# Optimization experiments

Hardware: AMD Instinct MI355X
Metric: run time of the kernel (lower is better)

Reference implementation:

```python
import jax, jax.numpy as jnp
import numpy as np

# Standard SMPL kinematic tree parents (kintree_table)
PARENTS = np.array([-1, 0, 0, 0, 1, 2, 3, 4, 5, 6, 7, 8, 9, 9, 9,
                    12, 13, 14, 16, 17, 18, 19, 20, 21])
NV, NJ, NB, NP = 6890, 24, 10, 207


def rodrigues(r):
    """Axis-angle [N,3] -> rotation matrices [N,3,3] (Rodrigues formula)."""
    theta = jnp.linalg.norm(r, axis=1, keepdims=True) + 1e-8  # [N,1]
    rh = r / theta                                            # [N,3]
    cos = jnp.cos(theta)[..., None]                           # [N,1,1]
    sin = jnp.sin(theta)[..., None]
    z = jnp.zeros_like(rh[:, 0])
    m = jnp.stack([z, -rh[:, 2], rh[:, 1],
                   rh[:, 2], z, -rh[:, 0],
                   -rh[:, 1], rh[:, 0], z], axis=1).reshape(-1, 3, 3)
    dot = rh[:, :, None] * rh[:, None, :]                     # outer product
    eye = jnp.eye(3, dtype=r.dtype)
    return cos * eye + (1.0 - cos) * dot + sin * m


def setup_inputs() -> dict:
    key = jax.random.key(0)
    ks = jax.random.split(key, 9)
    B = 512
    betas = jax.random.normal(ks[0], (B, NB), dtype=jnp.float32)
    thetas = jax.random.normal(ks[1], (B, NJ * 3), dtype=jnp.float32) * 0.3
    trans = jax.random.normal(ks[2], (B, 3), dtype=jnp.float32)
    scale = jnp.ones((1,), dtype=jnp.float32)
    v_template = jax.random.normal(ks[3], (NV, 3), dtype=jnp.float32)
    shapedirs = jax.random.normal(ks[4], (NV, 3, NB), dtype=jnp.float32) * 0.01
    posedirs = jax.random.normal(ks[5], (NV, 3, NP), dtype=jnp.float32) * 0.01
    Jr = jax.random.uniform(ks[6], (NJ, NV), dtype=jnp.float32)
    J_regressor = Jr / jnp.sum(Jr, axis=1, keepdims=True)
    w = jax.random.uniform(ks[7], (NV, NJ), dtype=jnp.float32)
    weights = w / jnp.sum(w, axis=1, keepdims=True)
    return {"betas": betas, "thetas": thetas, "trans": trans, "scale": scale,
            "v_template": v_template, "shapedirs": shapedirs,
            "posedirs": posedirs, "J_regressor": J_regressor,
            "weights": weights}


def reference(betas, thetas, trans, scale, v_template, shapedirs, posedirs,
              J_regressor, weights):
    B = betas.shape[0]
    dt = betas.dtype
    # Shape blend shapes: v_shaped [B, 6890, 3]
    v_shaped = jnp.einsum('bs,vcs->bvc', betas, shapedirs) + v_template
    # Rest-pose joints J(beta): [B, 24, 3]
    J = jnp.einsum('jv,bvc->bjc', J_regressor, v_shaped)
    # Local rotations from axis-angle, root scaled by `scale`
    lRs = rodrigues(thetas.reshape(-1, 3)).reshape(B, NJ, 3, 3)
    lRs = lRs.at[:, 0].multiply(scale[0])
    # Local joint offsets: root keeps J[:,0], children use J[i] - J[parent[i]]
    parents = jnp.asarray(PARENTS)
    t = J - J[:, jnp.clip(parents, 0)]
    t = t.at[:, 0].set(J[:, 0])
    # Local 4x4 transforms [B, 24, 4, 4]
    top = jnp.concatenate([lRs, t[..., None]], axis=3)          # [B,24,3,4]
    bottom = jnp.broadcast_to(jnp.array([0., 0., 0., 1.], dtype=dt),
                              (B, NJ, 1, 4))
    A = jnp.concatenate([top, bottom], axis=2)
    # Kinematic chain accumulation (fixed 24-joint tree)
    results = [A[:, 0]]
    for i in range(1, NJ):
        results.append(results[PARENTS[i]] @ A[:, i])
    stacked = jnp.stack(results, axis=1)                         # [B,24,4,4]
    # Remove rest-pose joint locations from translation column
    Jh = jnp.concatenate([J, jnp.zeros((B, NJ, 1), dtype=dt)], axis=2)
    deformed = jnp.einsum('bjxy,bjy->bjx', stacked, Jh)          # [B,24,4]
    G = stacked.at[..., 3].add(-deformed)
    # Pose blend shapes from non-root rotations
    lrotmin = (lRs[:, 1:] - jnp.eye(3, dtype=dt)).reshape(B, -1)  # [B,207]
    v_posed = v_shaped + jnp.einsum('bp,vcp->bvc', lrotmin, posedirs)
    # Linear blend skinning
    T = jnp.einsum('bjxy,vj->bvxy', G, weights)                  # [B,6890,4,4]
    vh = jnp.concatenate([v_posed, jnp.ones((B, NV, 1), dtype=dt)], axis=2)
    v = jnp.einsum('bvxy,bvy->bvx', T, vh)[:, :, :3]
    result = v + trans[:, None, :]
    joints = jnp.einsum('jv,bvc->bjc', J_regressor, result)
    return result, joints
```

## Files before the change

kernel.cpp:

```cpp
#include <hip/hip_runtime.h>

#define NVERT 6890
#define NJNT  24
#define NBETA 10
#define NPOSE 207
#define NBATCH 512
#define KPAD 224
#define MROWS 20736
#define NVC (NVERT * 3)

typedef __attribute__((ext_vector_type(8))) short short8;
typedef __attribute__((ext_vector_type(4))) float floatx4;

__constant__ int c_par[NJNT]   = {-1,0,0,0,1,2,3,4,5,6,7,8,9,9,9,12,13,14,16,17,18,19,20,21};
__constant__ int c_depth[NJNT] = { 0,1,1,1,2,2,2,3,3,3,4,4,4,4,4,5,5,5,6,6,7,7,8,8};

static __device__ __forceinline__ unsigned short f2bf(float x) {
  union { float f; unsigned u; } v; v.f = x;
  unsigned r = (v.u + 0x7FFFu + ((v.u >> 16) & 1u)) >> 16;
  return (unsigned short)r;
}
static __device__ __forceinline__ float bf2f(unsigned short h) {
  union { unsigned u; float f; } v; v.u = (unsigned)h << 16;
  return v.f;
}

__global__ __launch_bounds__(256) void k_buildA(
    const float* __restrict__ pdir, const float* __restrict__ sd,
    const float* __restrict__ vt, unsigned short* __restrict__ AT) {
  const int idx = blockIdx.x * 256 + threadIdx.x;
  const int kk = idx & 31;
  const int row = (idx >> 5) % MROWS;
  const int kt = idx / (MROWS * 32);
  const int k = kt * 32 + kk;
  float val = 0.f;
  if (row < NVC) {
    if (k < NPOSE)            val = pdir[(size_t)row * NPOSE + k];
    else if (k < NPOSE + 10)  val = sd[(size_t)row * 10 + (k - NPOSE)];
    else if (k == NPOSE + 10) val = vt[row];
  }
  AT[idx] = f2bf(val);
}

__global__ __launch_bounds__(256) void k_buildW(
    const float* __restrict__ wgt, unsigned short* __restrict__ W16) {
  const int idx = blockIdx.x * 256 + threadIdx.x;
  const int v = idx >> 6, c = idx & 63, j = c & 31, h = c >> 5;
  const float w = (v < NVERT && j < 24) ? wgt[(size_t)v * 24 + j] : 0.f;
  const unsigned short hi = f2bf(w);
  W16[idx] = h ? f2bf(w - bf2f(hi)) : hi;
}

__global__ __launch_bounds__(256) void k_jreg1(
    const float* __restrict__ Jr, const float* __restrict__ vt,
    const float* __restrict__ sd, float* __restrict__ wsJP) {
  const int jc = blockIdx.x, j = jc / 3, c = jc % 3;
  const int v0 = blockIdx.y * 864;
  const int vend = min(NVERT, v0 + 864);
  const int tid = threadIdx.x;
  float acc[11];
  #pragma unroll
  for (int k = 0; k < 11; ++k) acc[k] = 0.f;
  for (int v = v0 + tid; v < vend; v += 256) {
    const float w = Jr[j * NVERT + v];
    acc[0] += w * vt[v * 3 + c];
    const float* s = sd + (size_t)v * 30 + c * 10;
    #pragma unroll
    for (int k = 0; k < 10; ++k) acc[1 + k] += w * s[k];
  }
  #pragma unroll
  for (int off = 32; off > 0; off >>= 1) {
    #pragma unroll
    for (int k = 0; k < 11; ++k) acc[k] += __shfl_down(acc[k], off, 64);
  }
  __shared__ float red[4][11];
  const int lane = tid & 63, wv = tid >> 6;
  if (lane == 0) {
    #pragma unroll
    for (int k = 0; k < 11; ++k) red[wv][k] = acc[k];
  }
  __syncthreads();
  if (tid == 0) {
    #pragma unroll
    for (int k = 0; k < 11; ++k)
      wsJP[(size_t)(blockIdx.y * 72 + jc) * 11 + k] =
          red[0][k] + red[1][k] + red[2][k] + red[3][k];
  }
}

__global__ __launch_bounds__(256, 2) void k_chain3(
    const float* __restrict__ betas, const float* __restrict__ thetas,
    const float* __restrict__ scale, const float* __restrict__ trans,
    const float* __restrict__ wsJP,
    unsigned short* __restrict__ BT, unsigned short* __restrict__ G16) {
  __shared__ __align__(16) float sJ[792];
  __shared__ __align__(16) float sJJ[4][72];
  __shared__ __align__(16) float sM[4][288];
  __shared__ __align__(16) unsigned short sG[4][1024];
  __shared__ __align__(16) unsigned short sB[4][KPAD];

  const int tid = threadIdx.x;
  const int wv = tid >> 6, lane = tid & 63;
  const int b = blockIdx.x * 4 + wv;

  if (tid < 72) {
    #pragma unroll
    for (int k = 0; k < 11; ++k) {
      float s = 0.f;
      #pragma unroll
      for (int c8 = 0; c8 < 8; ++c8) s += wsJP[(size_t)(c8 * 72 + tid) * 11 + k];
      if (k == 0) sJ[tid] = s;
      else        sJ[72 + tid * 10 + (k - 1)] = s;
    }
  }
  #pragma unroll
  for (int r = 0; r < 4; ++r) {
    sG[wv][lane * 16 + r * 4 + 0] = 0; sG[wv][lane * 16 + r * 4 + 1] = 0;
    sG[wv][lane * 16 + r * 4 + 2] = 0; sG[wv][lane * 16 + r * 4 + 3] = 0;
  }
  __syncthreads();

  float R[9], t[3], M[12], Jx = 0.f, Jy = 0.f, Jz = 0.f;
  const int i = lane;
  if (i < NJNT) {
    #pragma unroll
    for (int c = 0; c < 3; ++c) {
      float a = sJ[i * 3 + c];
      const float* d = sJ + 72 + (i * 3 + c) * 10;
      #pragma unroll
      for (int s = 0; s < NBETA; ++s) a += d[s] * betas[b * NBETA + s];
      if (c == 0) Jx = a; else if (c == 1) Jy = a; else Jz = a;
    }
    sJJ[wv][i * 3 + 0] = Jx; sJJ[wv][i * 3 + 1] = Jy; sJJ[wv][i * 3 + 2] = Jz;
    const float rx = thetas[b * 72 + i * 3 + 0];
    const float ry = thetas[b * 72 + i * 3 + 1];
    const float rz = thetas[b * 72 + i * 3 + 2];
    const float th = sqrtf(rx * rx + ry * ry + rz * rz) + 1e-8f;
    const float inv = 1.f / th;
    const float x = rx * inv, y = ry * inv, z = rz * inv;
    const float cs = cosf(th), sn = sinf(th), omc = 1.f - cs;
    R[0] = cs + omc * x * x;     R[1] = omc * x * y - sn * z; R[2] = omc * x * z + sn * y;
    R[3] = omc * x * y + sn * z; R[4] = cs + omc * y * y;     R[5] = omc * y * z - sn * x;
    R[6] = omc * x * z - sn * y; R[7] = omc * y * z + sn * x; R[8] = cs + omc * z * z;
    if (i == 0) {
      const float sc = scale[0];
      #pragma unroll
      for (int k = 0; k < 9; ++k) R[k] *= sc;
    } else {
      #pragma unroll
      for (int k = 0; k < 9; ++k)
        sB[wv][(i - 1) * 9 + k] = f2bf(R[k] - ((k == 0 || k == 4 || k == 8) ? 1.f : 0.f));
    }
  }
  if (i == 0) {
    #pragma unroll
    for (int s = 0; s < NBETA; ++s) sB[wv][NPOSE + s] = f2bf(betas[b * NBETA + s]);
    sB[wv][NPOSE + 10] = 0x3F80;
    #pragma unroll
    for (int k = NPOSE + 11; k < KPAD; ++k) sB[wv][k] = 0;
  }
  __syncthreads();

  if (i < NJNT) {
    if (i == 0) { t[0] = Jx; t[1] = Jy; t[2] = Jz; }
    else {
      const int p = c_par[i];
      t[0] = Jx - sJJ[wv][p * 3 + 0];
      t[1] = Jy - sJJ[wv][p * 3 + 1];
      t[2] = Jz - sJJ[wv][p * 3 + 2];
    }
    if (i == 0) {
      #pragma unroll
      for (int r = 0; r < 3; ++r) {
        M[r*4+0] = R[r*3+0]; M[r*4+1] = R[r*3+1]; M[r*4+2] = R[r*3+2]; M[r*4+3] = t[r];
      }
      #pragma unroll
      for (int k = 0; k < 12; ++k) sM[wv][k] = M[k];
    }
  }
  __syncthreads();

  for (int lvl = 1; lvl <= 8; ++lvl) {
    if (i < NJNT && c_depth[i] == lvl) {
      const float* Mp = sM[wv] + c_par[i] * 12;
      #pragma unroll
      for (int r = 0; r < 3; ++r) {
        const float p0 = Mp[r*4+0], p1 = Mp[r*4+1], p2 = Mp[r*4+2], p3 = Mp[r*4+3];
        M[r*4+0] = p0*R[0] + p1*R[3] + p2*R[6];
        M[r*4+1] = p0*R[1] + p1*R[4] + p2*R[7];
        M[r*4+2] = p0*R[2] + p1*R[5] + p2*R[8];
        M[r*4+3] = p0*t[0] + p1*t[1] + p2*t[2] + p3;
      }
      #pragma unroll
      for (int k = 0; k < 12; ++k) sM[wv][i * 12 + k] = M[k];
    }
    __syncthreads();
  }

  if (i < NJNT) {
    #pragma unroll
    for (int r = 0; r < 3; ++r) {
      M[r*4+3] = M[r*4+3] - (M[r*4+0]*Jx + M[r*4+1]*Jy + M[r*4+2]*Jz)
               + trans[b * 3 + r];
    }
    #pragma unroll
    for (int e = 0; e < 12; ++e) {
      const float g = M[e];
      const unsigned short hi = f2bf(g);
      sG[wv][e * 32 + i]       = hi;
      sG[wv][512 + e * 32 + i] = f2bf(g - bf2f(hi));
    }
  }
  __syncthreads();

  *(uint4*)(G16 + (size_t)b * 1024 + lane * 16)     = *(uint4*)&sG[wv][lane * 16];
  *(uint4*)(G16 + (size_t)b * 1024 + lane * 16 + 8) = *(uint4*)&sG[wv][lane * 16 + 8];
  if (lane < 28)
    *(uint4*)(BT + ((size_t)(lane >> 2) * NBATCH + b) * 32 + (lane & 3) * 8) =
        *(uint4*)&sB[wv][lane * 8];
}

__global__ __launch_bounds__(256, 3) void k_skin4(
    const unsigned short* __restrict__ AT, const unsigned short* __restrict__ BT,
    const unsigned short* __restrict__ W16, const unsigned short* __restrict__ G16,
    float* __restrict__ out) {
  __shared__ __align__(16) char smem[33536];
  unsigned short* sAs = (unsigned short*)smem;
  unsigned short* sBs = (unsigned short*)(smem + 15360);
  float* sV           = (float*)smem;
  unsigned short* sG2 = (unsigned short*)(smem + 13056);

  const int tid = threadIdx.x;
  const int wv = tid >> 6, lane = tid & 63;
  const int q = lane >> 4, n = lane & 15;

  const int fb = blockIdx.x;
  const int vb = (fb & 7) * 108 + (fb >> 3);
  const int b0 = (vb & 7) * 64;
  const int by = vb >> 3;
  const int vc0 = by * 192;

  floatx4 acc[3][4];
  #pragma unroll
  for (int mt = 0; mt < 3; ++mt)
    #pragma unroll
    for (int nt = 0; nt < 4; ++nt) acc[mt][nt] = (floatx4)(0.f);

  const int srow = tid >> 2, sj = tid & 3;

  for (int kt = 0; kt < 7; ++kt) {
    if (kt) __syncthreads();
    #pragma unroll
    for (int it = 0; it < 3; ++it)
      *(uint4*)(sAs + (it * 64 + srow) * 40 + sj * 8) =
          *(const uint4*)(AT + ((size_t)kt * MROWS + vc0 + it * 64 + srow) * 32 + sj * 8);
    *(uint4*)(sBs + srow * 40 + sj * 8) =
        *(const uint4*)(BT + ((size_t)kt * NBATCH + b0 + srow) * 32 + sj * 8);
    __syncthreads();
    short8 af[3], bfr[4];
    #pragma unroll
    for (int mt = 0; mt < 3; ++mt)
      af[mt] = *(const short8*)(sAs + (48 * wv + 16 * mt + n) * 40 + q * 8);
    #pragma unroll
    for (int nt = 0; nt < 4; ++nt)
      bfr[nt] = *(const short8*)(sBs + (16 * nt + n) * 40 + q * 8);
    #pragma unroll
    for (int mt = 0; mt < 3; ++mt)
      #pragma unroll
      for (int nt = 0; nt < 4; ++nt)
        acc[mt][nt] = __builtin_amdgcn_mfma_f32_16x16x32_bf16(
            af[mt], bfr[nt], acc[mt][nt], 0, 0, 0);
  }

  short8 wh[4], wl[4];
  #pragma unroll
  for (int vt = 0; vt < 4; ++vt) {
    const unsigned short* wr = W16 + (size_t)(by * 64 + vt * 16 + n) * 64;
    wh[vt] = *(const short8*)(wr + q * 8);
    wl[vt] = *(const short8*)(wr + 32 + q * 8);
  }

  for (int nt = 0; nt < 4; ++nt) {
    for (int s = 0; s < 2; ++s) {
      __syncthreads();
      if (s == 0) {
        #pragma unroll
        for (int mt = 0; mt < 3; ++mt)
          #pragma unroll
          for (int r = 0; r < 4; ++r)
            sV[(48 * wv + 16 * mt + 4 * q + r) * 17 + n] = acc[mt][nt][r];
      }
      const int bg0 = b0 + nt * 16 + s * 8;
      for (int i = tid; i < 1024; i += 256) {
        const int row = i >> 2, c4 = i & 3;
        const int t = row >> 5, rem = row & 31;
        *(uint4*)(sG2 + row * 40 + c4 * 8) =
            *(const uint4*)(G16 + (size_t)(bg0 + t) * 1024 + rem * 32 + c4 * 8);
      }
      __syncthreads();
      #pragma unroll
      for (int bb = 0; bb < 2; ++bb) {
        const int t = wv * 2 + bb;
        const int col = s * 8 + t;
        const int bg = b0 + nt * 16 + col;
        const short8 gh = *(const short8*)(sG2 + (t * 32 + n) * 40 + q * 8);
        const short8 gl = *(const short8*)(sG2 + (t * 32 + 16 + n) * 40 + q * 8);
        #pragma unroll
        for (int vt = 0; vt < 4; ++vt) {
          floatx4 a2 = (floatx4)(0.f);
          a2 = __builtin_amdgcn_mfma_f32_16x16x32_bf16(gh, wl[vt], a2, 0, 0, 0);
          a2 = __builtin_amdgcn_mfma_f32_16x16x32_bf16(gl, wh[vt], a2, 0, 0, 0);
          a2 = __builtin_amdgcn_mfma_f32_16x16x32_bf16(gh, wh[vt], a2, 0, 0, 0);
          const float X = sV[(48 * vt + 3 * n + 0) * 17 + col];
          const float Y = sV[(48 * vt + 3 * n + 1) * 17 + col];
          const float Z = sV[(48 * vt + 3 * n + 2) * 17 + col];
          const float o = a2[0] * X + a2[1] * Y + a2[2] * Z + a2[3];
          const int vc = vc0 + 48 * vt + 3 * n + q;
          if (q < 3 && vc < NVC)
            out[(size_t)bg * NVC + vc] = o;
        }
      }
    }
  }
}

__global__ __launch_bounds__(256) void k_jnt1(
    const float* __restrict__ Jr, const float* __restrict__ res,
    float* __restrict__ wsJ2) {
  const int b0 = blockIdx.x * 2;
  const int chunk = blockIdx.y;
  const int v0 = chunk * 864;
  const int vend = min(NVERT, v0 + 864);
  const int lane = threadIdx.x & 63, wv = threadIdx.x >> 6;
  float acc[36];
  #pragma unroll
  for (int k = 0; k < 36; ++k) acc[k] = 0.f;
  const float* rA = res + (size_t)b0 * NVC;
  const float* rB = res + (size_t)(b0 + 1) * NVC;
  for (int v = v0 + lane; v < vend; v += 64) {
    const float a0 = rA[v * 3 + 0], a1 = rA[v * 3 + 1], a2 = rA[v * 3 + 2];
    const float e0 = rB[v * 3 + 0], e1 = rB[v * 3 + 1], e2 = rB[v * 3 + 2];
    #pragma unroll
    for (int k = 0; k < 6; ++k) {
      const int j = wv + 4 * k;
      const float w = Jr[j * NVERT + v];
      acc[k*6+0] += w * a0; acc[k*6+1] += w * a1; acc[k*6+2] += w * a2;
      acc[k*6+3] += w * e0; acc[k*6+4] += w * e1; acc[k*6+5] += w * e2;
    }
  }
  #pragma unroll
  for (int off = 32; off > 0; off >>= 1) {
    #pragma unroll
    for (int k = 0; k < 36; ++k) acc[k] += __shfl_down(acc[k], off, 64);
  }
  if (lane == 0) {
    #pragma unroll
    for (int k = 0; k < 6; ++k) {
      const int j = wv + 4 * k;
      float* d0 = wsJ2 + ((size_t)b0 * 8 + chunk) * 72 + j * 3;
      d0[0] = acc[k*6+0]; d0[1] = acc[k*6+1]; d0[2] = acc[k*6+2];
      float* d1 = wsJ2 + ((size_t)(b0 + 1) * 8 + chunk) * 72 + j * 3;
      d1[0] = acc[k*6+3]; d1[1] = acc[k*6+4]; d1[2] = acc[k*6+5];
    }
  }
}

__global__ __launch_bounds__(256) void k_jnt2(
    const float* __restrict__ wsJ2, float* __restrict__ joints) {
  const int idx = blockIdx.x * 256 + threadIdx.x;
  const int b = idx / 72, jc = idx - b * 72;
  float s = 0.f;
  #pragma unroll
  for (int c8 = 0; c8 < 8; ++c8)
    s += wsJ2[((size_t)b * 8 + c8) * 72 + jc];
  joints[idx] = s;
}

extern "C" void kernel_launch(void* const* d_in, const int* in_sizes, int n_in,
                              void* d_out, int out_size, void* d_ws, size_t ws_size,
                              hipStream_t stream) {
  const float* betas  = (const float*)d_in[0];
  const float* thetas = (const float*)d_in[1];
  const float* trans  = (const float*)d_in[2];
  const float* scale  = (const float*)d_in[3];
  const float* vtpl   = (const float*)d_in[4];
  const float* sd     = (const float*)d_in[5];
  const float* pdir   = (const float*)d_in[6];
  const float* Jr     = (const float*)d_in[7];
  const float* wgt    = (const float*)d_in[8];
  float* out = (float*)d_out;

  float* ws   = (float*)d_ws;
  float* wsJP = ws;
  unsigned short* AT  = (unsigned short*)(ws + 6336);
  unsigned short* BT  = AT + (size_t)MROWS * KPAD;
  unsigned short* W16 = BT + (size_t)NBATCH * KPAD;
  unsigned short* G16 = W16 + (size_t)6912 * 64;
  float* wsJ2 = (float*)AT;

  k_buildA<<<(MROWS * KPAD) / 256, 256, 0, stream>>>(pdir, sd, vtpl, AT);
  k_buildW<<<(6912 * 64) / 256, 256, 0, stream>>>(wgt, W16);
  k_jreg1<<<dim3(72, 8), 256, 0, stream>>>(Jr, vtpl, sd, wsJP);
  k_chain3<<<NBATCH / 4, 256, 0, stream>>>(betas, thetas, scale, trans, wsJP, BT, G16);
  k_skin4<<<864, 256, 0, stream>>>(AT, BT, W16, G16, out);
  k_jnt1<<<dim3(NBATCH / 2, 8), 256, 0, stream>>>(Jr, out, wsJ2);
  k_jnt2<<<(NBATCH * 72) / 256, 256, 0, stream>>>(wsJ2, out + (size_t)NBATCH * NVC);
}
```

Before: 171.5 us.

## Merge prep kernels into one launch and register-prefetch skin kernel tiles

The three preparation kernels (bf16 conversion of the blend-shape matrix, split-bf16 skinning weights, joint-regressor partial sums) become one launch whose block ranges select the task. This removes two launches and lets the independent tasks run concurrently. In the skinning kernel, the A/B K-tiles and the G transform tiles are now prefetched into registers one step ahead, so global loads overlap the MFMA work. The cost is higher register pressure, which may lower occupancy.

```diff
diff --git a/kernel.cpp b/kernel.cpp
--- a/kernel.cpp
+++ b/kernel.cpp
@@ -9,6 +9,10 @@
 #define MROWS 20736
 #define NVC (NVERT * 3)
 
+#define NBA 18144
+#define NBW 1728
+#define NJR 576
+
 typedef __attribute__((ext_vector_type(8))) short short8;
 typedef __attribute__((ext_vector_type(4))) float floatx4;
 
@@ -25,66 +29,67 @@
   return v.f;
 }
 
-__global__ __launch_bounds__(256) void k_buildA(
+__global__ __launch_bounds__(256) void k_prep(
     const float* __restrict__ pdir, const float* __restrict__ sd,
-    const float* __restrict__ vt, unsigned short* __restrict__ AT) {
-  const int idx = blockIdx.x * 256 + threadIdx.x;
-  const int kk = idx & 31;
-  const int row = (idx >> 5) % MROWS;
-  const int kt = idx / (MROWS * 32);
-  const int k = kt * 32 + kk;
-  float val = 0.f;
-  if (row < NVC) {
-    if (k < NPOSE)            val = pdir[(size_t)row * NPOSE + k];
-    else if (k < NPOSE + 10)  val = sd[(size_t)row * 10 + (k - NPOSE)];
-    else if (k == NPOSE + 10) val = vt[row];
-  }
-  AT[idx] = f2bf(val);
-}
-
-__global__ __launch_bounds__(256) void k_buildW(
-    const float* __restrict__ wgt, unsigned short* __restrict__ W16) {
-  const int idx = blockIdx.x * 256 + threadIdx.x;
-  const int v = idx >> 6, c = idx & 63, j = c & 31, h = c >> 5;
-  const float w = (v < NVERT && j < 24) ? wgt[(size_t)v * 24 + j] : 0.f;
-  const unsigned short hi = f2bf(w);
-  W16[idx] = h ? f2bf(w - bf2f(hi)) : hi;
-}
-
-__global__ __launch_bounds__(256) void k_jreg1(
-    const float* __restrict__ Jr, const float* __restrict__ vt,
-    const float* __restrict__ sd, float* __restrict__ wsJP) {
-  const int jc = blockIdx.x, j = jc / 3, c = jc % 3;
-  const int v0 = blockIdx.y * 864;
-  const int vend = min(NVERT, v0 + 864);
+    const float* __restrict__ vt, const float* __restrict__ wgt,
+    const float* __restrict__ Jr,
+    unsigned short* __restrict__ AT, unsigned short* __restrict__ W16,
+    float* __restrict__ wsJP) {
+  const int bx = blockIdx.x;
   const int tid = threadIdx.x;
-  float acc[11];
-  #pragma unroll
-  for (int k = 0; k < 11; ++k) acc[k] = 0.f;
-  for (int v = v0 + tid; v < vend; v += 256) {
-    const float w = Jr[j * NVERT + v];
-    acc[0] += w * vt[v * 3 + c];
-    const float* s = sd + (size_t)v * 30 + c * 10;
-    #pragma unroll
-    for (int k = 0; k < 10; ++k) acc[1 + k] += w * s[k];
-  }
-  #pragma unroll
-  for (int off = 32; off > 0; off >>= 1) {
-    #pragma unroll
-    for (int k = 0; k < 11; ++k) acc[k] += __shfl_down(acc[k], off, 64);
-  }
-  __shared__ float red[4][11];
-  const int lane = tid & 63, wv = tid >> 6;
-  if (lane == 0) {
-    #pragma unroll
-    for (int k = 0; k < 11; ++k) red[wv][k] = acc[k];
-  }
-  __syncthreads();
-  if (tid == 0) {
-    #pragma unroll
-    for (int k = 0; k < 11; ++k)
-      wsJP[(size_t)(blockIdx.y * 72 + jc) * 11 + k] =
-          red[0][k] + red[1][k] + red[2][k] + red[3][k];
+  if (bx < NBA) {
+    const int idx = bx * 256 + tid;
+    const int kk = idx & 31;
+    const int row = (idx >> 5) % MROWS;
+    const int kt = idx / (MROWS * 32);
+    const int k = kt * 32 + kk;
+    float val = 0.f;
+    if (row < NVC) {
+      if (k < NPOSE)            val = pdir[(size_t)row * NPOSE + k];
+      else if (k < NPOSE + 10)  val = sd[(size_t)row * 10 + (k - NPOSE)];
+      else if (k == NPOSE + 10) val = vt[row];
+    }
+    AT[idx] = f2bf(val);
+  } else if (bx < NBA + NBW) {
+    const int idx = (bx - NBA) * 256 + tid;
+    const int v = idx >> 6, c = idx & 63, j = c & 31;
+    const float w = (v < NVERT && j < 24) ? wgt[(size_t)v * 24 + j] : 0.f;
+    const unsigned short hi = f2bf(w);
+    W16[idx] = (c >> 5) ? f2bf(w - bf2f(hi)) : hi;
+  } else {
+    const int jb = bx - (NBA + NBW);
+    const int jc = jb % 72, j = jc / 3, c = jc % 3;
+    const int chunk = jb / 72;
+    const int v0 = chunk * 864;
+    const int vend = min(NVERT, v0 + 864);
+    float acc[11];
+    #pragma unroll
+    for (int k = 0; k < 11; ++k) acc[k] = 0.f;
+    for (int v = v0 + tid; v < vend; v += 256) {
+      const float w = Jr[j * NVERT + v];
+      acc[0] += w * vt[v * 3 + c];
+      const float* s = sd + (size_t)v * 30 + c * 10;
+      #pragma unroll
+      for (int k = 0; k < 10; ++k) acc[1 + k] += w * s[k];
+    }
+    #pragma unroll
+    for (int off = 32; off > 0; off >>= 1) {
+      #pragma unroll
+      for (int k = 0; k < 11; ++k) acc[k] += __shfl_down(acc[k], off, 64);
+    }
+    __shared__ float red[4][11];
+    const int lane = tid & 63, wv = tid >> 6;
+    if (lane == 0) {
+      #pragma unroll
+      for (int k = 0; k < 11; ++k) red[wv][k] = acc[k];
+    }
+    __syncthreads();
+    if (tid == 0) {
+      #pragma unroll
+      for (int k = 0; k < 11; ++k)
+        wsJP[(size_t)(chunk * 72 + jc) * 11 + k] =
+            red[0][k] + red[1][k] + red[2][k] + red[3][k];
+    }
   }
 }
 
@@ -248,15 +253,26 @@
 
   const int srow = tid >> 2, sj = tid & 3;
 
+  uint4 ra[3], rbq;
+  #pragma unroll
+  for (int it = 0; it < 3; ++it)
+    ra[it] = *(const uint4*)(AT + (size_t)(vc0 + it * 64 + srow) * 32 + sj * 8);
+  rbq = *(const uint4*)(BT + (size_t)(b0 + srow) * 32 + sj * 8);
+
   for (int kt = 0; kt < 7; ++kt) {
     if (kt) __syncthreads();
     #pragma unroll
     for (int it = 0; it < 3; ++it)
-      *(uint4*)(sAs + (it * 64 + srow) * 40 + sj * 8) =
-          *(const uint4*)(AT + ((size_t)kt * MROWS + vc0 + it * 64 + srow) * 32 + sj * 8);
-    *(uint4*)(sBs + srow * 40 + sj * 8) =
-        *(const uint4*)(BT + ((size_t)kt * NBATCH + b0 + srow) * 32 + sj * 8);
+      *(uint4*)(sAs + (it * 64 + srow) * 40 + sj * 8) = ra[it];
+    *(uint4*)(sBs + srow * 40 + sj * 8) = rbq;
     __syncthreads();
+    if (kt < 6) {
+      #pragma unroll
+      for (int it = 0; it < 3; ++it)
+        ra[it] = *(const uint4*)(AT +
+            ((size_t)(kt + 1) * MROWS + vc0 + it * 64 + srow) * 32 + sj * 8);
+      rbq = *(const uint4*)(BT + ((size_t)(kt + 1) * NBATCH + b0 + srow) * 32 + sj * 8);
+    }
     short8 af[3], bfr[4];
     #pragma unroll
     for (int mt = 0; mt < 3; ++mt)
@@ -278,6 +294,15 @@
     const unsigned short* wr = W16 + (size_t)(by * 64 + vt * 16 + n) * 64;
     wh[vt] = *(const short8*)(wr + q * 8);
     wl[vt] = *(const short8*)(wr + 32 + q * 8);
+  }
+
+  uint4 gr[4];
+  #pragma unroll
+  for (int c = 0; c < 4; ++c) {
+    const int i = tid + c * 256;
+    const int row = i >> 2, c4 = i & 3;
+    const int t = row >> 5, rem = row & 31;
+    gr[c] = *(const uint4*)(G16 + (size_t)(b0 + t) * 1024 + rem * 32 + c4 * 8);
   }
 
   for (int nt = 0; nt < 4; ++nt) {
@@ -290,14 +315,24 @@
           for (int r = 0; r < 4; ++r)
             sV[(48 * wv + 16 * mt + 4 * q + r) * 17 + n] = acc[mt][nt][r];
       }
-      const int bg0 = b0 + nt * 16 + s * 8;
-      for (int i = tid; i < 1024; i += 256) {
+      #pragma unroll
+      for (int c = 0; c < 4; ++c) {
+        const int i = tid + c * 256;
         const int row = i >> 2, c4 = i & 3;
-        const int t = row >> 5, rem = row & 31;
-        *(uint4*)(sG2 + row * 40 + c4 * 8) =
-            *(const uint4*)(G16 + (size_t)(bg0 + t) * 1024 + rem * 32 + c4 * 8);
+        *(uint4*)(sG2 + row * 40 + c4 * 8) = gr[c];
       }
       __syncthreads();
+      const int rnd = nt * 2 + s;
+      if (rnd < 7) {
+        const int bg0n = b0 + ((rnd + 1) >> 1) * 16 + ((rnd + 1) & 1) * 8;
+        #pragma unroll
+        for (int c = 0; c < 4; ++c) {
+          const int i = tid + c * 256;
+          const int row = i >> 2, c4 = i & 3;
+          const int t = row >> 5, rem = row & 31;
+          gr[c] = *(const uint4*)(G16 + (size_t)(bg0n + t) * 1024 + rem * 32 + c4 * 8);
+        }
+      }
       #pragma unroll
       for (int bb = 0; bb < 2; ++bb) {
         const int t = wv * 2 + bb;
@@ -398,9 +433,7 @@
   unsigned short* G16 = W16 + (size_t)6912 * 64;
   float* wsJ2 = (float*)AT;
 
-  k_buildA<<<(MROWS * KPAD) / 256, 256, 0, stream>>>(pdir, sd, vtpl, AT);
-  k_buildW<<<(6912 * 64) / 256, 256, 0, stream>>>(wgt, W16);
-  k_jreg1<<<dim3(72, 8), 256, 0, stream>>>(Jr, vtpl, sd, wsJP);
+  k_prep<<<NBA + NBW + NJR, 256, 0, stream>>>(pdir, sd, vtpl, wgt, Jr, AT, W16, wsJP);
   k_chain3<<<NBATCH / 4, 256, 0, stream>>>(betas, thetas, scale, trans, wsJP, BT, G16);
   k_skin4<<<864, 256, 0, stream>>>(AT, BT, W16, G16, out);
   k_jnt1<<<dim3(NBATCH / 2, 8), 256, 0, stream>>>(Jr, out, wsJ2);
```

New measurement: 213.6 us. 1.25x slower.
